# Optimization experiments

Hardware: AMD Instinct MI355X
Metric: run time of the kernel (lower is better)

Reference implementation:

```python
import jax, jax.numpy as jnp
import numpy as np

QMAX = 7.0            # int4 narrow range: [-7, 7]
SCALING_MIN_VAL = 2e-16


def fake_quant_weight_per_channel(w):
    """Brevitas CommonIntWeightPerChannelQuant, bit_width=4.

    Per-output-channel float scale from abs-max stats, narrow-range signed
    int4 round+clamp, then dequantize. STE so gradients pass through.
    w: [O, I, KH, KW]
    """
    amax = jnp.max(jnp.abs(w), axis=(1, 2, 3), keepdims=True)   # [O,1,1,1]
    scale = jnp.maximum(amax / QMAX, SCALING_MIN_VAL)
    wq = jnp.clip(jnp.round(w / scale), -QMAX, QMAX) * scale
    # straight-through estimator (matches Brevitas round_ste backward)
    return w + jax.lax.stop_gradient(wq - w)


def setup_inputs() -> dict:
    key = jax.random.key(0)
    kx, kw = jax.random.split(key)
    x = jax.random.normal(kx, (32, 256, 56, 56), dtype=jnp.float32)
    # conv weight [out_channels, in_channels, kh, kw]
    w = jax.random.normal(kw, (256, 256, 3, 3), dtype=jnp.float32) * 0.05
    return {"x": x, "w": w}


def reference(x, w):
    wq = fake_quant_weight_per_channel(w)
    return jax.lax.conv_general_dilated(
        x, wq,
        window_strides=(1, 1),
        padding=((1, 1), (1, 1)),
        dimension_numbers=("NCHW", "OIHW", "NCHW"),
    )
```

## Files before the change

kernel.cpp:

```cpp
#include <hip/hip_runtime.h>
#include <cstdint>
#include <cstddef>

typedef __bf16 bf16x8 __attribute__((ext_vector_type(8)));
typedef float  f32x4  __attribute__((ext_vector_type(4)));
typedef float  f32x16 __attribute__((ext_vector_type(16)));
typedef int    i32x4  __attribute__((ext_vector_type(4)));

#define QMAX 7.0f
#define SCALE_MIN 2e-16f

#define BAR()     asm volatile("s_barrier" ::: "memory")
#define WAITVM(N) asm volatile("s_waitcnt vmcnt(" #N ")" ::: "memory")

__global__ __launch_bounds__(256) void quant_w_kernel(const float* __restrict__ w,
                                                      __bf16* __restrict__ wq) {
    const int o = blockIdx.x;
    const int t = threadIdx.x;
    const float* wo = w + (size_t)o * 2304;

    float vals[9];
    float m = 0.f;
    #pragma unroll
    for (int i = 0; i < 9; ++i) {
        float v = wo[t + i * 256];
        vals[i] = v;
        m = fmaxf(m, fabsf(v));
    }
    #pragma unroll
    for (int off = 32; off >= 1; off >>= 1) m = fmaxf(m, __shfl_down(m, off));
    __shared__ float red[4];
    __shared__ float s_scale;
    if ((t & 63) == 0) red[t >> 6] = m;
    __syncthreads();
    if (t == 0) {
        float am = fmaxf(fmaxf(red[0], red[1]), fmaxf(red[2], red[3]));
        s_scale = fmaxf(am / QMAX, SCALE_MIN);
    }
    __syncthreads();
    const float scale = s_scale;

    #pragma unroll
    for (int i = 0; i < 9; ++i) {
        int idx = t + i * 256;
        int c = idx / 9;
        int tap = idx - c * 9;
        float q = rintf(vals[i] / scale);
        q = fminf(QMAX, fmaxf(-QMAX, q));
        wq[(size_t)tap * 65536 + (size_t)o * 256 + c] = (__bf16)(q * scale);
    }
}

__global__ __launch_bounds__(256) void convert_x_kernel(const float* __restrict__ x,
                                                        __bf16* __restrict__ xpad) {
    __shared__ float tile[32][33];
    const int n  = blockIdx.z;
    const int c0 = blockIdx.y * 32;
    const int p0 = blockIdx.x * 32;
    const int tx = threadIdx.x & 31;
    const int ty = threadIdx.x >> 5;

    #pragma unroll
    for (int r = 0; r < 4; ++r) {
        int c = c0 + ty + r * 8;
        tile[ty + r * 8][tx] = x[((size_t)(n * 256 + c)) * 3136 + p0 + tx];
    }
    __syncthreads();
    #pragma unroll
    for (int r = 0; r < 4; ++r) {
        int p = p0 + ty + r * 8;
        int h = p / 56, wcol = p - h * 56;
        xpad[(((size_t)n * 58 + h + 1) * 58 + (wcol + 1)) * 256 + c0 + tx] =
            (__bf16)tile[tx][ty + r * 8];
    }
}

__global__ __launch_bounds__(256) void zero_halo_kernel(__bf16* __restrict__ xpad) {
    const int t = blockIdx.x * 256 + threadIdx.x;
    const int cvec = t & 31;
    const int r    = t >> 5;
    const int n    = r / 228;
    const int pos  = r - n * 228;
    if (n >= 32) return;
    int h, wcol;
    if      (pos < 58)  { h = 0;          wcol = pos; }
    else if (pos < 116) { h = 57;         wcol = pos - 58; }
    else if (pos < 172) { h = pos - 115;  wcol = 0; }
    else                { h = pos - 171;  wcol = 57; }
    i32x4* dst = (i32x4*)(xpad + (((size_t)n * 58 + h) * 58 + wcol) * 256);
    dst[cvec] = (i32x4){0, 0, 0, 0};
}

__device__ __forceinline__ void gload_lds16(const void* g, void* l) {
    __builtin_amdgcn_global_load_lds((const __attribute__((address_space(1))) void*)g,
                                     (__attribute__((address_space(3))) void*)l,
                                     16, 0, 0);
}

__global__ __launch_bounds__(512, 2) void conv_mfma_kernel(const __bf16* __restrict__ xpad,
                                                           const __bf16* __restrict__ wq,
                                                           float* __restrict__ out) {
    extern __shared__ __align__(16) char lds[];
    const int tid  = threadIdx.x;
    const int wv   = tid >> 6;
    const int lane = tid & 63;
    const int bid  = blockIdx.x;
    const int swz  = (bid & 7) * 49 + (bid >> 3);
    const int p0   = swz * 256;

    const int wr = wv >> 2;
    const int wc = wv & 3;

    const int schunk = (lane & 7) ^ (lane >> 3);
    const int srowA = (wv >> 2) * 128 + (wv & 3) * 8 + (lane >> 3);
    const __bf16* pAg = wq + (size_t)srowA * 256 + schunk * 8;
    const int srowB = (wv >> 1) * 64 + (wv & 1) * 8 + (lane >> 3);
    const __bf16* pB[4];
    #pragma unroll
    for (int j = 0; j < 4; ++j) {
        int pos = p0 + srowB + j * 16;
        int ni = pos / 3136;
        int hw = pos - ni * 3136;
        int h = hw / 56, w = hw - h * 56;
        pB[j] = xpad + (((size_t)ni * 58 + h) * 58 + w) * 256 + schunk * 8;
    }
    const int adst = ((wv >> 2) * 128 + (wv & 3) * 8) * 128;
    const int bdst = ((wv >> 1) * 64  + (wv & 1) * 8) * 128;

    const int hi = lane >> 5;
    int kxo[4];
    #pragma unroll
    for (int ks = 0; ks < 4; ++ks)
        kxo[ks] = ((ks * 2 + hi) ^ (lane & 7)) * 16;
    const int arowb = (wr * 128 + (lane & 31)) * 128;
    const int browb = (wc * 64  + (lane & 31)) * 128;

    f32x16 acc[4][2];
    #pragma unroll
    for (int m = 0; m < 4; ++m)
        #pragma unroll
        for (int n = 0; n < 2; ++n)
            acc[m][n] = (f32x16)(0.f);

    {
        char* Aw = lds;
        char* Bw = lds + 32768;
        gload_lds16(pAg + 0 * 8192, Aw + adst + 0 * 4096);
        gload_lds16(pB[0],          Bw + bdst + 0 * 2048);
        gload_lds16(pAg + 1 * 8192, Aw + adst + 1 * 4096);
        gload_lds16(pB[1],          Bw + bdst + 1 * 2048);
        gload_lds16(pB[2],          Bw + bdst + 2 * 2048);
        gload_lds16(pB[3],          Bw + bdst + 3 * 2048);
        gload_lds16(pAg + 2 * 8192, Aw + adst + 2 * 4096);
        gload_lds16(pAg + 3 * 8192, Aw + adst + 3 * 4096);
    }

    for (int s = 0; s < 36; ++s) {
        const int cur = s & 1;
        const char* Ard = lds + (cur ? 65536 : 0);
        const char* Brd = Ard + 32768;
        char* Awr = lds + (cur ? 0 : 65536);
        char* Bwr = Awr + 32768;
        const bool stg = (s < 35);
        size_t aoffN = 0, boffN = 0;
        if (stg) {
            const int sn = s + 1;
            const int tapN = sn >> 2, ccN = sn & 3;
            const int khN = tapN / 3, kwN = tapN - khN * 3;
            aoffN = (size_t)tapN * 65536 + ccN * 64;
            boffN = (size_t)(khN * 58 + kwN) * 256 + ccN * 64;
        }

        bf16x8 a0[4], a1[4], b0[4], b1[4];

        WAITVM(4);
        BAR();
        #pragma unroll
        for (int ks = 0; ks < 4; ++ks) {
            a0[ks] = *(const bf16x8*)(Ard + arowb + 0 * 4096 + kxo[ks]);
            a1[ks] = *(const bf16x8*)(Ard + arowb + 1 * 4096 + kxo[ks]);
            b0[ks] = *(const bf16x8*)(Brd + browb + 0 * 4096 + kxo[ks]);
        }
        if (stg) {
            gload_lds16(pAg + 0 * 8192 + aoffN, Awr + adst + 0 * 4096);
            gload_lds16(pB[0] + boffN,          Bwr + bdst + 0 * 2048);
            gload_lds16(pAg + 1 * 8192 + aoffN, Awr + adst + 1 * 4096);
            gload_lds16(pB[1] + boffN,          Bwr + bdst + 1 * 2048);
        }
        __builtin_amdgcn_s_setprio(1);
        #pragma unroll
        for (int ks = 0; ks < 4; ++ks) {
            acc[0][0] = __builtin_amdgcn_mfma_f32_32x32x16_bf16(a0[ks], b0[ks], acc[0][0], 0, 0, 0);
            acc[1][0] = __builtin_amdgcn_mfma_f32_32x32x16_bf16(a1[ks], b0[ks], acc[1][0], 0, 0, 0);
        }
        __builtin_amdgcn_s_setprio(0);
        BAR();

        if (stg) { WAITVM(6); } else { WAITVM(2); }
        BAR();
        #pragma unroll
        for (int ks = 0; ks < 4; ++ks)
            b1[ks] = *(const bf16x8*)(Brd + browb + 1 * 4096 + kxo[ks]);
        if (stg) {
            gload_lds16(pB[2] + boffN, Bwr + bdst + 2 * 2048);
            gload_lds16(pB[3] + boffN, Bwr + bdst + 3 * 2048);
        }
        __builtin_amdgcn_s_setprio(1);
        #pragma unroll
        for (int ks = 0; ks < 4; ++ks) {
            acc[0][1] = __builtin_amdgcn_mfma_f32_32x32x16_bf16(a0[ks], b1[ks], acc[0][1], 0, 0, 0);
            acc[1][1] = __builtin_amdgcn_mfma_f32_32x32x16_bf16(a1[ks], b1[ks], acc[1][1], 0, 0, 0);
        }
        __builtin_amdgcn_s_setprio(0);
        BAR();

        if (stg) { WAITVM(6); } else { WAITVM(0); }
        BAR();
        #pragma unroll
        for (int ks = 0; ks < 4; ++ks) {
            a0[ks] = *(const bf16x8*)(Ard + arowb + 2 * 4096 + kxo[ks]);
            a1[ks] = *(const bf16x8*)(Ard + arowb + 3 * 4096 + kxo[ks]);
        }
        if (stg) {
            gload_lds16(pAg + 2 * 8192 + aoffN, Awr + adst + 2 * 4096);
            gload_lds16(pAg + 3 * 8192 + aoffN, Awr + adst + 3 * 4096);
        }
        __builtin_amdgcn_s_setprio(1);
        #pragma unroll
        for (int ks = 0; ks < 4; ++ks) {
            acc[2][0] = __builtin_amdgcn_mfma_f32_32x32x16_bf16(a0[ks], b0[ks], acc[2][0], 0, 0, 0);
            acc[3][0] = __builtin_amdgcn_mfma_f32_32x32x16_bf16(a1[ks], b0[ks], acc[3][0], 0, 0, 0);
        }
        __builtin_amdgcn_s_setprio(0);
        BAR();

        __builtin_amdgcn_s_setprio(1);
        #pragma unroll
        for (int ks = 0; ks < 4; ++ks) {
            acc[2][1] = __builtin_amdgcn_mfma_f32_32x32x16_bf16(a0[ks], b1[ks], acc[2][1], 0, 0, 0);
            acc[3][1] = __builtin_amdgcn_mfma_f32_32x32x16_bf16(a1[ks], b1[ks], acc[3][1], 0, 0, 0);
        }
        __builtin_amdgcn_s_setprio(0);
        BAR();
    }

    #pragma unroll
    for (int n = 0; n < 2; ++n) {
        const int pos = p0 + wc * 64 + n * 32 + (lane & 31);
        const int ni = pos / 3136;
        const int hw = pos - ni * 3136;
        float* ob = out + (size_t)ni * 802816 + hw;
        #pragma unroll
        for (int m = 0; m < 4; ++m) {
            const int om = wr * 128 + m * 32 + 4 * hi;
            #pragma unroll
            for (int r = 0; r < 16; ++r) {
                const int o = om + (r & 3) + 8 * (r >> 2);
                ob[(size_t)o * 3136] = acc[m][n][r];
            }
        }
    }
}

__global__ __launch_bounds__(256) void conv_naive_kernel(const float* __restrict__ x,
                                                         const float* __restrict__ w,
                                                         float* __restrict__ out) {
    const int n = blockIdx.z;
    const int o = blockIdx.y;
    const int strip = blockIdx.x;
    __shared__ float wqs[2304];
    __shared__ float red[4];
    __shared__ float s_scale;
    const float* wo = w + (size_t)o * 2304;
    float m = 0.f;
    for (int i = threadIdx.x; i < 2304; i += 256) m = fmaxf(m, fabsf(wo[i]));
    #pragma unroll
    for (int off = 32; off >= 1; off >>= 1) m = fmaxf(m, __shfl_down(m, off));
    if ((threadIdx.x & 63) == 0) red[threadIdx.x >> 6] = m;
    __syncthreads();
    if (threadIdx.x == 0) {
        float am = fmaxf(fmaxf(red[0], red[1]), fmaxf(red[2], red[3]));
        s_scale = fmaxf(am / QMAX, SCALE_MIN);
    }
    __syncthreads();
    const float scale = s_scale;
    for (int i = threadIdx.x; i < 2304; i += 256) {
        float q = rintf(wo[i] / scale);
        q = fminf(QMAX, fmaxf(-QMAX, q));
        wqs[i] = q * scale;
    }
    __syncthreads();
    int p = strip * 256 + threadIdx.x;
    if (p >= 3136) return;
    int h = p / 56, wcol = p - h * 56;
    float acc = 0.f;
    for (int c = 0; c < 256; ++c) {
        const float* xc = x + ((size_t)(n * 256 + c)) * 3136;
        const float* wk = wqs + c * 9;
        #pragma unroll
        for (int kh = 0; kh < 3; ++kh) {
            int hh = h + kh - 1;
            if (hh < 0 || hh > 55) continue;
            #pragma unroll
            for (int kw = 0; kw < 3; ++kw) {
                int ww2 = wcol + kw - 1;
                if (ww2 < 0 || ww2 > 55) continue;
                acc += xc[hh * 56 + ww2] * wk[kh * 3 + kw];
            }
        }
    }
    out[((size_t)(n * 256 + o)) * 3136 + p] = acc;
}

extern "C" void kernel_launch(void* const* d_in, const int* in_sizes, int n_in,
                              void* d_out, int out_size, void* d_ws, size_t ws_size,
                              hipStream_t stream) {
    const float* x = (const float*)d_in[0];
    const float* w = (const float*)d_in[1];
    float* out = (float*)d_out;

    const size_t WQ_BYTES   = 9ull * 256 * 256 * 2;
    const size_t XPAD_OFF   = WQ_BYTES;
    const size_t XPAD_BYTES = 32ull * 58 * 58 * 256 * 2;

    if (ws_size >= XPAD_OFF + XPAD_BYTES) {
        __bf16* wq   = (__bf16*)d_ws;
        __bf16* xpad = (__bf16*)((char*)d_ws + XPAD_OFF);
        hipFuncSetAttribute((const void*)conv_mfma_kernel,
                            hipFuncAttributeMaxDynamicSharedMemorySize, 131072);
        zero_halo_kernel<<<912, 256, 0, stream>>>(xpad);
        quant_w_kernel<<<256, 256, 0, stream>>>(w, wq);
        convert_x_kernel<<<dim3(98, 8, 32), 256, 0, stream>>>(x, xpad);
        conv_mfma_kernel<<<392, 512, 131072, stream>>>(xpad, wq, out);
    } else {
        conv_naive_kernel<<<dim3(13, 256, 32), 256, 0, stream>>>(x, w, out);
    }
}
```

Baseline: 173.2 us.

## Shrink conv MFMA tile to 128x128 with 256-thread blocks and 64KB LDS

Reduces the implicit-GEMM block tile from 256 output channels x 256 positions (512 threads, 128KB LDS) to 128x128 (256 threads, 64KB LDS). Each block now covers half the output channels, giving 1568 blocks instead of 392. The per-stage schedule drops from four compute phases to two. The aim is better occupancy and load balance across CUs. In exchange each input tile is loaded twice, so global and LDS traffic per FLOP goes up.

```diff
diff --git a/kernel.cpp b/kernel.cpp
--- a/kernel.cpp
+++ b/kernel.cpp
@@ -97,7 +97,7 @@
                                      16, 0, 0);
 }
 
-__global__ __launch_bounds__(512, 2) void conv_mfma_kernel(const __bf16* __restrict__ xpad,
+__global__ __launch_bounds__(256, 2) void conv_mfma_kernel(const __bf16* __restrict__ xpad,
                                                            const __bf16* __restrict__ wq,
                                                            float* __restrict__ out) {
     extern __shared__ __align__(16) char lds[];
@@ -105,62 +105,60 @@
     const int wv   = tid >> 6;
     const int lane = tid & 63;
     const int bid  = blockIdx.x;
-    const int swz  = (bid & 7) * 49 + (bid >> 3);
-    const int p0   = swz * 256;
-
-    const int wr = wv >> 2;
-    const int wc = wv & 3;
+    const int swz  = (bid & 7) * 196 + (bid >> 3);
+    const int ptile = swz >> 1;
+    const int ohalf = swz & 1;
+    const int p0   = ptile * 128;
+    const int o0   = ohalf * 128;
+
+    const int wm = wv >> 1;
+    const int wn = wv & 1;
 
     const int schunk = (lane & 7) ^ (lane >> 3);
-    const int srowA = (wv >> 2) * 128 + (wv & 3) * 8 + (lane >> 3);
-    const __bf16* pAg = wq + (size_t)srowA * 256 + schunk * 8;
-    const int srowB = (wv >> 1) * 64 + (wv & 1) * 8 + (lane >> 3);
+    const __bf16* pAg = wq + (size_t)(o0 + wv * 8 + (lane >> 3)) * 256 + schunk * 8;
     const __bf16* pB[4];
     #pragma unroll
     for (int j = 0; j < 4; ++j) {
-        int pos = p0 + srowB + j * 16;
+        int row = (wv & 1) * 64 + (j >> 1) * 32 + (j & 1) * 16 + (wv >> 1) * 8 + (lane >> 3);
+        int pos = p0 + row;
         int ni = pos / 3136;
         int hw = pos - ni * 3136;
         int h = hw / 56, w = hw - h * 56;
         pB[j] = xpad + (((size_t)ni * 58 + h) * 58 + w) * 256 + schunk * 8;
     }
-    const int adst = ((wv >> 2) * 128 + (wv & 3) * 8) * 128;
-    const int bdst = ((wv >> 1) * 64  + (wv & 1) * 8) * 128;
+    const int adst = wv * 1024;
+    const int bdst = 16384 + (wv & 1) * 8192 + (wv >> 1) * 1024;
 
     const int hi = lane >> 5;
     int kxo[4];
     #pragma unroll
     for (int ks = 0; ks < 4; ++ks)
         kxo[ks] = ((ks * 2 + hi) ^ (lane & 7)) * 16;
-    const int arowb = (wr * 128 + (lane & 31)) * 128;
-    const int browb = (wc * 64  + (lane & 31)) * 128;
-
-    f32x16 acc[4][2];
-    #pragma unroll
-    for (int m = 0; m < 4; ++m)
+    const int arowb = (wm * 64 + (lane & 31)) * 128;
+    const int browb = 16384 + (wn * 64 + (lane & 31)) * 128;
+
+    f32x16 acc[2][2];
+    #pragma unroll
+    for (int m = 0; m < 2; ++m)
         #pragma unroll
         for (int n = 0; n < 2; ++n)
             acc[m][n] = (f32x16)(0.f);
 
     {
-        char* Aw = lds;
-        char* Bw = lds + 32768;
-        gload_lds16(pAg + 0 * 8192, Aw + adst + 0 * 4096);
-        gload_lds16(pB[0],          Bw + bdst + 0 * 2048);
-        gload_lds16(pAg + 1 * 8192, Aw + adst + 1 * 4096);
-        gload_lds16(pB[1],          Bw + bdst + 1 * 2048);
-        gload_lds16(pB[2],          Bw + bdst + 2 * 2048);
-        gload_lds16(pB[3],          Bw + bdst + 3 * 2048);
-        gload_lds16(pAg + 2 * 8192, Aw + adst + 2 * 4096);
-        gload_lds16(pAg + 3 * 8192, Aw + adst + 3 * 4096);
+        char* buf = lds;
+        gload_lds16(pAg + 0 * 8192, buf + adst + 0 * 4096);
+        gload_lds16(pAg + 1 * 8192, buf + adst + 1 * 4096);
+        gload_lds16(pAg + 2 * 8192, buf + adst + 2 * 4096);
+        gload_lds16(pAg + 3 * 8192, buf + adst + 3 * 4096);
+        gload_lds16(pB[0],          buf + bdst + 0 * 4096 + 0 * 2048);
+        gload_lds16(pB[1],          buf + bdst + 0 * 4096 + 1 * 2048);
+        gload_lds16(pB[2],          buf + bdst + 1 * 4096 + 0 * 2048);
+        gload_lds16(pB[3],          buf + bdst + 1 * 4096 + 1 * 2048);
     }
 
     for (int s = 0; s < 36; ++s) {
-        const int cur = s & 1;
-        const char* Ard = lds + (cur ? 65536 : 0);
-        const char* Brd = Ard + 32768;
-        char* Awr = lds + (cur ? 0 : 65536);
-        char* Bwr = Awr + 32768;
+        const char* Rd = lds + ((s & 1) ? 32768 : 0);
+        char*       Wr = lds + ((s & 1) ? 0 : 32768);
         const bool stg = (s < 35);
         size_t aoffN = 0, boffN = 0;
         if (stg) {
@@ -171,88 +169,60 @@
             boffN = (size_t)(khN * 58 + kwN) * 256 + ccN * 64;
         }
 
-        bf16x8 a0[4], a1[4], b0[4], b1[4];
-
-        WAITVM(4);
+        bf16x8 a0[4], a1[4], b[4];
+
+        WAITVM(2);
         BAR();
         #pragma unroll
         for (int ks = 0; ks < 4; ++ks) {
-            a0[ks] = *(const bf16x8*)(Ard + arowb + 0 * 4096 + kxo[ks]);
-            a1[ks] = *(const bf16x8*)(Ard + arowb + 1 * 4096 + kxo[ks]);
-            b0[ks] = *(const bf16x8*)(Brd + browb + 0 * 4096 + kxo[ks]);
+            a0[ks] = *(const bf16x8*)(Rd + arowb + 0 * 4096 + kxo[ks]);
+            a1[ks] = *(const bf16x8*)(Rd + arowb + 1 * 4096 + kxo[ks]);
+            b[ks]  = *(const bf16x8*)(Rd + browb + 0 * 4096 + kxo[ks]);
         }
         if (stg) {
-            gload_lds16(pAg + 0 * 8192 + aoffN, Awr + adst + 0 * 4096);
-            gload_lds16(pB[0] + boffN,          Bwr + bdst + 0 * 2048);
-            gload_lds16(pAg + 1 * 8192 + aoffN, Awr + adst + 1 * 4096);
-            gload_lds16(pB[1] + boffN,          Bwr + bdst + 1 * 2048);
+            gload_lds16(pAg + 0 * 8192 + aoffN, Wr + adst + 0 * 4096);
+            gload_lds16(pAg + 1 * 8192 + aoffN, Wr + adst + 1 * 4096);
+            gload_lds16(pAg + 2 * 8192 + aoffN, Wr + adst + 2 * 4096);
+            gload_lds16(pAg + 3 * 8192 + aoffN, Wr + adst + 3 * 4096);
+            gload_lds16(pB[0] + boffN,          Wr + bdst + 0 * 2048);
+            gload_lds16(pB[1] + boffN,          Wr + bdst + 2048);
         }
         __builtin_amdgcn_s_setprio(1);
         #pragma unroll
         for (int ks = 0; ks < 4; ++ks) {
-            acc[0][0] = __builtin_amdgcn_mfma_f32_32x32x16_bf16(a0[ks], b0[ks], acc[0][0], 0, 0, 0);
-            acc[1][0] = __builtin_amdgcn_mfma_f32_32x32x16_bf16(a1[ks], b0[ks], acc[1][0], 0, 0, 0);
+            acc[0][0] = __builtin_amdgcn_mfma_f32_32x32x16_bf16(a0[ks], b[ks], acc[0][0], 0, 0, 0);
+            acc[1][0] = __builtin_amdgcn_mfma_f32_32x32x16_bf16(a1[ks], b[ks], acc[1][0], 0, 0, 0);
+        }
+        __builtin_amdgcn_s_setprio(0);
+
+        if (stg) { WAITVM(6); } else { WAITVM(0); }
+        BAR();
+        #pragma unroll
+        for (int ks = 0; ks < 4; ++ks)
+            b[ks] = *(const bf16x8*)(Rd + browb + 1 * 4096 + kxo[ks]);
+        if (stg) {
+            gload_lds16(pB[2] + boffN, Wr + bdst + 4096);
+            gload_lds16(pB[3] + boffN, Wr + bdst + 4096 + 2048);
+        }
+        __builtin_amdgcn_s_setprio(1);
+        #pragma unroll
+        for (int ks = 0; ks < 4; ++ks) {
+            acc[0][1] = __builtin_amdgcn_mfma_f32_32x32x16_bf16(a0[ks], b[ks], acc[0][1], 0, 0, 0);
+            acc[1][1] = __builtin_amdgcn_mfma_f32_32x32x16_bf16(a1[ks], b[ks], acc[1][1], 0, 0, 0);
         }
         __builtin_amdgcn_s_setprio(0);
         BAR();
-
-        if (stg) { WAITVM(6); } else { WAITVM(2); }
-        BAR();
-        #pragma unroll
-        for (int ks = 0; ks < 4; ++ks)
-            b1[ks] = *(const bf16x8*)(Brd + browb + 1 * 4096 + kxo[ks]);
-        if (stg) {
-            gload_lds16(pB[2] + boffN, Bwr + bdst + 2 * 2048);
-            gload_lds16(pB[3] + boffN, Bwr + bdst + 3 * 2048);
-        }
-        __builtin_amdgcn_s_setprio(1);
-        #pragma unroll
-        for (int ks = 0; ks < 4; ++ks) {
-            acc[0][1] = __builtin_amdgcn_mfma_f32_32x32x16_bf16(a0[ks], b1[ks], acc[0][1], 0, 0, 0);
-            acc[1][1] = __builtin_amdgcn_mfma_f32_32x32x16_bf16(a1[ks], b1[ks], acc[1][1], 0, 0, 0);
-        }
-        __builtin_amdgcn_s_setprio(0);
-        BAR();
-
-        if (stg) { WAITVM(6); } else { WAITVM(0); }
-        BAR();
-        #pragma unroll
-        for (int ks = 0; ks < 4; ++ks) {
-            a0[ks] = *(const bf16x8*)(Ard + arowb + 2 * 4096 + kxo[ks]);
-            a1[ks] = *(const bf16x8*)(Ard + arowb + 3 * 4096 + kxo[ks]);
-        }
-        if (stg) {
-            gload_lds16(pAg + 2 * 8192 + aoffN, Awr + adst + 2 * 4096);
-            gload_lds16(pAg + 3 * 8192 + aoffN, Awr + adst + 3 * 4096);
-        }
-        __builtin_amdgcn_s_setprio(1);
-        #pragma unroll
-        for (int ks = 0; ks < 4; ++ks) {
-            acc[2][0] = __builtin_amdgcn_mfma_f32_32x32x16_bf16(a0[ks], b0[ks], acc[2][0], 0, 0, 0);
-            acc[3][0] = __builtin_amdgcn_mfma_f32_32x32x16_bf16(a1[ks], b0[ks], acc[3][0], 0, 0, 0);
-        }
-        __builtin_amdgcn_s_setprio(0);
-        BAR();
-
-        __builtin_amdgcn_s_setprio(1);
-        #pragma unroll
-        for (int ks = 0; ks < 4; ++ks) {
-            acc[2][1] = __builtin_amdgcn_mfma_f32_32x32x16_bf16(a0[ks], b1[ks], acc[2][1], 0, 0, 0);
-            acc[3][1] = __builtin_amdgcn_mfma_f32_32x32x16_bf16(a1[ks], b1[ks], acc[3][1], 0, 0, 0);
-        }
-        __builtin_amdgcn_s_setprio(0);
-        BAR();
     }
 
     #pragma unroll
     for (int n = 0; n < 2; ++n) {
-        const int pos = p0 + wc * 64 + n * 32 + (lane & 31);
+        const int pos = p0 + wn * 64 + n * 32 + (lane & 31);
         const int ni = pos / 3136;
         const int hw = pos - ni * 3136;
         float* ob = out + (size_t)ni * 802816 + hw;
         #pragma unroll
-        for (int m = 0; m < 4; ++m) {
-            const int om = wr * 128 + m * 32 + 4 * hi;
+        for (int m = 0; m < 2; ++m) {
+            const int om = o0 + wm * 64 + m * 32 + 4 * hi;
             #pragma unroll
             for (int r = 0; r < 16; ++r) {
                 const int o = om + (r & 3) + 8 * (r >> 2);
@@ -327,11 +297,11 @@
         __bf16* wq   = (__bf16*)d_ws;
         __bf16* xpad = (__bf16*)((char*)d_ws + XPAD_OFF);
         hipFuncSetAttribute((const void*)conv_mfma_kernel,
-                            hipFuncAttributeMaxDynamicSharedMemorySize, 131072);
+                            hipFuncAttributeMaxDynamicSharedMemorySize, 65536);
         zero_halo_kernel<<<912, 256, 0, stream>>>(xpad);
         quant_w_kernel<<<256, 256, 0, stream>>>(w, wq);
         convert_x_kernel<<<dim3(98, 8, 32), 256, 0, stream>>>(x, xpad);
-        conv_mfma_kernel<<<392, 512, 131072, stream>>>(xpad, wq, out);
+        conv_mfma_kernel<<<1568, 256, 65536, stream>>>(xpad, wq, out);
     } else {
         conv_naive_kernel<<<dim3(13, 256, 32), 256, 0, stream>>>(x, w, out);
     }
```

Result: no change. 174.8 us (+0.9%).
